# Optimization experiments

Measured on AMD Instinct MI355X. Metric: run time of the kernel, lower is better.

The kernel has to match this reference:

```python
import jax, jax.numpy as jnp
import numpy as np

D_MODEL = 512
N_HEADS = 8
HEAD_DIM = D_MODEL // N_HEADS
MAX_LEN = 250  # relative table has 2*MAX_LEN-1 = 499 rows
B, L = 2, 2048


def setup_inputs() -> dict:
    rng = jax.random.key(0)
    ks = jax.random.split(rng, 10)
    w = 1.0 / np.sqrt(D_MODEL)
    return {
        "query": jax.random.normal(ks[0], (B, L, D_MODEL), jnp.float32),
        "key": jax.random.normal(ks[1], (B, L, D_MODEL), jnp.float32),
        "value": jax.random.normal(ks[2], (B, L, D_MODEL), jnp.float32),
        "mask": jax.random.randint(ks[3], (B, L), 0, 2, jnp.int32),
        # weights stored as [in, out]; apply as x @ W + b (equivalent to torch Linear)
        "Wq": jax.random.normal(ks[4], (D_MODEL, D_MODEL), jnp.float32) * w,
        "bq": jnp.zeros((D_MODEL,), jnp.float32),
        "Wk": jax.random.normal(ks[5], (D_MODEL, D_MODEL), jnp.float32) * w,
        "bk": jnp.zeros((D_MODEL,), jnp.float32),
        "Wv": jax.random.normal(ks[6], (D_MODEL, D_MODEL), jnp.float32) * w,
        "bv": jnp.zeros((D_MODEL,), jnp.float32),
        "Wo": jax.random.normal(ks[7], (D_MODEL, D_MODEL), jnp.float32) * w,
        "bo": jnp.zeros((D_MODEL,), jnp.float32),
        "rel_table": jax.random.normal(ks[8], (2 * MAX_LEN - 1, HEAD_DIM), jnp.float32),
    }


def reference(query, key, value, mask, Wq, bq, Wk, bk, Wv, bv, Wo, bo, rel_table):
    b, l, d = query.shape
    hd = d // N_HEADS

    def split_heads(x):  # [b,l,d] -> [b,h,l,hd]
        return x.reshape(b, l, N_HEADS, hd).transpose(0, 2, 1, 3)

    Q = split_heads(query @ Wq + bq)
    K = split_heads(key @ Wk + bk)
    V = split_heads(value @ Wv + bv)

    scores = jnp.einsum('bhid,bhjd->bhij', Q, K) / jnp.sqrt(jnp.float32(hd))

    # relative position indices: idx[i,j] = clamp(j - i + MAX_LEN-1, 0, 2*MAX_LEN-2)
    pos = jnp.arange(l)
    idx = jnp.clip(pos[None, :] - pos[:, None] + MAX_LEN - 1, 0, 2 * MAX_LEN - 2)
    rel = rel_table[idx]  # [l, l, hd] gather
    # Shaw-style additive relative-position bias (per-pair scalar from Q . rel)
    scores = scores + jnp.einsum('bhid,ijd->bhij', Q, rel)

    # key-padding mask: [b,l] -> [b,1,1,l]
    scores = jnp.where(mask[:, None, None, :] == 0, jnp.float32(-1e10), scores)

    weights = jax.nn.softmax(scores, axis=-1)  # [b,h,l,l]
    out = jnp.einsum('bhij,bhjd->bhid', weights, V)
    out = out.transpose(0, 2, 1, 3).reshape(b, l, d)
    return out @ Wo + bo
```

## Files before the change

### kernel.cpp

```cpp
#include <hip/hip_runtime.h>
#include <math.h>

#define NREL 499
#define NREL_PAD 504
#define LDB 72
#define LDT 72

typedef __attribute__((ext_vector_type(8))) short bf16x8;
typedef __attribute__((ext_vector_type(4))) float f32x4;

__device__ __forceinline__ float bf2f(ushort x) {
  union { unsigned u; float f; } v; v.u = ((unsigned)x) << 16; return v.f;
}
__device__ __forceinline__ ushort f2bf(float x) {
  union { float f; unsigned u; } v; v.f = x;
  return (ushort)((v.u + 0x8000u) >> 16);
}
__device__ __forceinline__ ushort f2h(float x) {
  union { _Float16 h; ushort u; } v; v.h = (_Float16)x; return v.u;
}
__device__ __forceinline__ float h2f(ushort u) {
  union { _Float16 h; ushort u; } v; v.u = u; return (float)v.h;
}
__device__ __forceinline__ bf16x8 pack8(float4 a, float4 b) {
  bf16x8 r;
  r[0] = (short)f2bf(a.x); r[1] = (short)f2bf(a.y);
  r[2] = (short)f2bf(a.z); r[3] = (short)f2bf(a.w);
  r[4] = (short)f2bf(b.x); r[5] = (short)f2bf(b.y);
  r[6] = (short)f2bf(b.z); r[7] = (short)f2bf(b.w);
  return r;
}

__global__ __launch_bounds__(256) void prep_wt(const float* __restrict__ W0,
                                               const float* __restrict__ W1,
                                               const float* __restrict__ W2,
                                               const float* __restrict__ W3,
                                               const int* __restrict__ mask,
                                               const float* __restrict__ rel,
                                               ushort* __restrict__ Wt,
                                               ushort* __restrict__ maskbf,
                                               ushort* __restrict__ rel8) {
  __shared__ float T[64][68];
  const int t = threadIdx.x;
  const int k0 = blockIdx.x * 64, n0 = blockIdx.y * 64, z = blockIdx.z;
  const float* W = (z == 0) ? W0 : (z == 1) ? W1 : (z == 2) ? W2 : W3;
#pragma unroll
  for (int s = 0; s < 4; ++s) {
    int idx = t + s * 256;
    int r = idx >> 4, c4 = (idx & 15) << 2;
    *(float4*)&T[r][c4] = *(const float4*)(W + (size_t)(k0 + r) * 512 + n0 + c4);
  }
  if (blockIdx.x == 0 && blockIdx.y == 0) {
    int base = z * 1024 + t * 4;
    int4 mv = *(const int4*)(mask + base);
    ushort4 mo;
    mo.x = mv.x ? 0x3F80 : 0; mo.y = mv.y ? 0x3F80 : 0;
    mo.z = mv.z ? 0x3F80 : 0; mo.w = mv.w ? 0x3F80 : 0;
    *(ushort4*)(maskbf + base) = mo;
  } else if (blockIdx.x == 1 && blockIdx.y == 0) {
    int base = z * 8192 + t * 32;
#pragma unroll
    for (int c = 0; c < 4; ++c) {
      int e0 = base + c * 8;
      ushort tmp[8];
#pragma unroll
      for (int k = 0; k < 8; ++k) {
        int e = e0 + k;
        float v = (e < NREL * 64) ? rel[e] * 8.f : 0.f;
        tmp[k] = f2bf(v);
      }
      *(ushort4*)(rel8 + e0) = make_ushort4(tmp[0], tmp[1], tmp[2], tmp[3]);
      *(ushort4*)(rel8 + e0 + 4) = make_ushort4(tmp[4], tmp[5], tmp[6], tmp[7]);
    }
  }
  __syncthreads();
#pragma unroll
  for (int s = 0; s < 4; ++s) {
    int idx = t + s * 256;
    int row = idx >> 4, c4 = (idx & 15) << 2;
    ushort4 u = make_ushort4(f2bf(T[c4 + 0][row]), f2bf(T[c4 + 1][row]),
                             f2bf(T[c4 + 2][row]), f2bf(T[c4 + 3][row]));
    *(ushort4*)(Wt + (size_t)z * 262144 + (size_t)(n0 + row) * 512 + k0 + c4) = u;
  }
}

template <int MODE, int AFP32>
__device__ __forceinline__ void gemm_tile_body(const void* __restrict__ Av,
                                               const ushort* __restrict__ Wt,
                                               const float* __restrict__ bias,
                                               const int* __restrict__ mvec,
                                               void* __restrict__ outv,
                                               int bx, int by, float oscale) {
  __shared__ ushort As[64 * LDT];
  __shared__ ushort Bs[64 * LDT];
  const int t = threadIdx.x;
  const int lane = t & 63, wave = t >> 6;
  const int m16 = lane & 15, quad = lane >> 4;
  const int koff = quad << 3;
  const int i0 = by * 64, n0 = bx * 64;
  const int row0 = t >> 3, off0 = (t & 7) << 3;
  const int row1 = (t + 256) >> 3, off1 = ((t + 256) & 7) << 3;
  const ushort* Ab16 = (const ushort*)Av + (size_t)i0 * 512;
  const float*  Ab32 = (const float*)Av + (size_t)i0 * 512;
  const ushort* Bb = Wt + (size_t)n0 * 512;

  uint4 ar0, ar1;
  float4 af00, af01, af10, af11;
  if (AFP32) {
    af00 = *(const float4*)(Ab32 + (size_t)row0 * 512 + off0);
    af01 = *(const float4*)(Ab32 + (size_t)row0 * 512 + off0 + 4);
    af10 = *(const float4*)(Ab32 + (size_t)row1 * 512 + off1);
    af11 = *(const float4*)(Ab32 + (size_t)row1 * 512 + off1 + 4);
  } else {
    ar0 = *(const uint4*)(Ab16 + (size_t)row0 * 512 + off0);
    ar1 = *(const uint4*)(Ab16 + (size_t)row1 * 512 + off1);
  }
  uint4 br0 = *(const uint4*)(Bb + (size_t)row0 * 512 + off0);
  uint4 br1 = *(const uint4*)(Bb + (size_t)row1 * 512 + off1);

  f32x4 acc[4] = {{0.f, 0.f, 0.f, 0.f}, {0.f, 0.f, 0.f, 0.f},
                  {0.f, 0.f, 0.f, 0.f}, {0.f, 0.f, 0.f, 0.f}};

  for (int ks = 0; ks < 8; ++ks) {
    __syncthreads();
    if (AFP32) {
      *(bf16x8*)&As[row0 * LDT + off0] = pack8(af00, af01);
      *(bf16x8*)&As[row1 * LDT + off1] = pack8(af10, af11);
    } else {
      *(uint4*)&As[row0 * LDT + off0] = ar0;
      *(uint4*)&As[row1 * LDT + off1] = ar1;
    }
    *(uint4*)&Bs[row0 * LDT + off0] = br0;
    *(uint4*)&Bs[row1 * LDT + off1] = br1;
    __syncthreads();

    const int kn = ((ks + 1) & 7) << 6;
    if (AFP32) {
      af00 = *(const float4*)(Ab32 + (size_t)row0 * 512 + kn + off0);
      af01 = *(const float4*)(Ab32 + (size_t)row0 * 512 + kn + off0 + 4);
      af10 = *(const float4*)(Ab32 + (size_t)row1 * 512 + kn + off1);
      af11 = *(const float4*)(Ab32 + (size_t)row1 * 512 + kn + off1 + 4);
    } else {
      ar0 = *(const uint4*)(Ab16 + (size_t)row0 * 512 + kn + off0);
      ar1 = *(const uint4*)(Ab16 + (size_t)row1 * 512 + kn + off1);
    }
    br0 = *(const uint4*)(Bb + (size_t)row0 * 512 + kn + off0);
    br1 = *(const uint4*)(Bb + (size_t)row1 * 512 + kn + off1);

    __builtin_amdgcn_s_setprio(1);
    if (MODE != 1) {
#pragma unroll
      for (int kh = 0; kh < 2; ++kh) {
        bf16x8 af = *(const bf16x8*)&As[((wave << 4) + m16) * LDT + (kh << 5) + koff];
#pragma unroll
        for (int nt = 0; nt < 4; ++nt) {
          bf16x8 wf = *(const bf16x8*)&Bs[((nt << 4) + m16) * LDT + (kh << 5) + koff];
          acc[nt] = __builtin_amdgcn_mfma_f32_16x16x32_bf16(af, wf, acc[nt], 0, 0, 0);
        }
      }
    } else {
#pragma unroll
      for (int kh = 0; kh < 2; ++kh) {
        bf16x8 wf = *(const bf16x8*)&Bs[((wave << 4) + m16) * LDT + (kh << 5) + koff];
#pragma unroll
        for (int it = 0; it < 4; ++it) {
          bf16x8 af = *(const bf16x8*)&As[((it << 4) + m16) * LDT + (kh << 5) + koff];
          acc[it] = __builtin_amdgcn_mfma_f32_16x16x32_bf16(wf, af, acc[it], 0, 0, 0);
        }
      }
    }
    __builtin_amdgcn_s_setprio(0);
  }

  if (MODE == 0) {
    float* out = (float*)outv;
#pragma unroll
    for (int nt = 0; nt < 4; ++nt) {
      float bn = bias[n0 + (nt << 4) + m16];
#pragma unroll
      for (int r = 0; r < 4; ++r) {
        int i = i0 + (wave << 4) + (quad << 2) + r;
        out[(size_t)i * 512 + n0 + (nt << 4) + m16] = acc[nt][r] + bn;
      }
    }
  } else {
    ushort* out = (ushort*)outv;
    const int b = i0 >> 11, l0 = i0 & 2047, h = n0 >> 6;
    float4 b4 = *(const float4*)(bias + n0 + (wave << 4) + (quad << 2));
    float bb[4] = {b4.x, b4.y, b4.z, b4.w};
    float mkf[4];
#pragma unroll
    for (int it = 0; it < 4; ++it)
      mkf[it] = (mvec[b * 2048 + l0 + (it << 4) + m16] != 0) ? 1.f : 0.f;
#pragma unroll
    for (int r = 0; r < 4; ++r) {
      int d = (wave << 4) + (quad << 2) + r;
#pragma unroll
      for (int it = 0; it < 4; ++it) {
        out[((size_t)(b * 8 + h) * 64 + d) * 2048 + l0 + (it << 4) + m16] =
            f2bf((acc[it][r] + bb[r]) * mkf[it]);
      }
    }
  }
}

template <int MODE, int AFP32>
__global__ __launch_bounds__(256) void gemm_tile(const void* __restrict__ A,
                                                 const ushort* __restrict__ Wt,
                                                 const float* __restrict__ bias,
                                                 void* __restrict__ outv) {
  gemm_tile_body<MODE, AFP32>(A, Wt, bias, nullptr, outv, blockIdx.x,
                              blockIdx.y, 1.f);
}

template <int QREL>
__device__ __forceinline__ void gemm_qk128(const float* __restrict__ A,
                                           const ushort* __restrict__ Wt,
                                           const float* __restrict__ bias,
                                           ushort* __restrict__ out,
                                           const ushort* __restrict__ rel8,
                                           ushort* __restrict__ qrelh,
                                           int bx, int by, float oscale) {
  __shared__ ushort As[128 * LDT];
  __shared__ ushort Bs[64 * LDT];
  const int t = threadIdx.x;
  const int lane = t & 63, wave = t >> 6;
  const int m16 = lane & 15, quad = lane >> 4;
  const int koff = quad << 3;
  const int i0 = by * 128, n0 = bx * 64;
  const float* Ab = A + (size_t)i0 * 512;
  const ushort* Bb = Wt + (size_t)n0 * 512;

  int arow[4], acol[4];
#pragma unroll
  for (int s = 0; s < 4; ++s) {
    int idx = t + s * 256;
    arow[s] = idx >> 3;
    acol[s] = (idx & 7) << 3;
  }
  const int brow0 = t >> 3, bcol0 = (t & 7) << 3;
  const int brow1 = (t + 256) >> 3, bcol1 = ((t + 256) & 7) << 3;

  float4 afA[4], afB[4];
  uint4 br0, br1;
#pragma unroll
  for (int s = 0; s < 4; ++s) {
    afA[s] = *(const float4*)(Ab + (size_t)arow[s] * 512 + acol[s]);
    afB[s] = *(const float4*)(Ab + (size_t)arow[s] * 512 + acol[s] + 4);
  }
  br0 = *(const uint4*)(Bb + (size_t)brow0 * 512 + bcol0);
  br1 = *(const uint4*)(Bb + (size_t)brow1 * 512 + bcol1);

  f32x4 acc[2][4];
#pragma unroll
  for (int mi = 0; mi < 2; ++mi)
#pragma unroll
    for (int nt = 0; nt < 4; ++nt) acc[mi][nt] = (f32x4){0.f, 0.f, 0.f, 0.f};

  for (int ks = 0; ks < 8; ++ks) {
    __syncthreads();
#pragma unroll
    for (int s = 0; s < 4; ++s)
      *(bf16x8*)&As[arow[s] * LDT + acol[s]] = pack8(afA[s], afB[s]);
    *(uint4*)&Bs[brow0 * LDT + bcol0] = br0;
    *(uint4*)&Bs[brow1 * LDT + bcol1] = br1;
    __syncthreads();

    const int kn = ((ks + 1) & 7) << 6;
#pragma unroll
    for (int s = 0; s < 4; ++s) {
      afA[s] = *(const float4*)(Ab + (size_t)arow[s] * 512 + kn + acol[s]);
      afB[s] = *(const float4*)(Ab + (size_t)arow[s] * 512 + kn + acol[s] + 4);
    }
    br0 = *(const uint4*)(Bb + (size_t)brow0 * 512 + kn + bcol0);
    br1 = *(const uint4*)(Bb + (size_t)brow1 * 512 + kn + bcol1);

    __builtin_amdgcn_s_setprio(1);
#pragma unroll
    for (int kh = 0; kh < 2; ++kh) {
      bf16x8 af0 = *(const bf16x8*)&As[((wave << 5) + m16) * LDT + (kh << 5) + koff];
      bf16x8 af1 = *(const bf16x8*)&As[((wave << 5) + 16 + m16) * LDT + (kh << 5) + koff];
#pragma unroll
      for (int nt = 0; nt < 4; ++nt) {
        bf16x8 wf = *(const bf16x8*)&Bs[((nt << 4) + m16) * LDT + (kh << 5) + koff];
        acc[0][nt] = __builtin_amdgcn_mfma_f32_16x16x32_bf16(af0, wf, acc[0][nt], 0, 0, 0);
        acc[1][nt] = __builtin_amdgcn_mfma_f32_16x16x32_bf16(af1, wf, acc[1][nt], 0, 0, 0);
      }
    }
    __builtin_amdgcn_s_setprio(0);
  }

  const int b = i0 >> 11, l0 = i0 & 2047, h = n0 >> 6;
#pragma unroll
  for (int nt = 0; nt < 4; ++nt) {
    float bn = bias[n0 + (nt << 4) + m16];
    int d = (nt << 4) + m16;
#pragma unroll
    for (int mi = 0; mi < 2; ++mi) {
#pragma unroll
      for (int r = 0; r < 4; ++r) {
        int il = (wave << 5) + (mi << 4) + (quad << 2) + r;
        ushort qb = f2bf((acc[mi][nt][r] + bn) * oscale);
        out[((size_t)(b * 8 + h) * 2048 + l0 + il) * 64 + d] = qb;
        if (QREL) As[il * LDT + d] = qb;
      }
    }
  }

  if (QREL) {
    __asm__ volatile("s_waitcnt lgkmcnt(0)" ::: "memory");
    bf16x8 afq[2][2];
#pragma unroll
    for (int g = 0; g < 2; ++g)
#pragma unroll
      for (int kh = 0; kh < 2; ++kh)
        afq[g][kh] = *(const bf16x8*)&As[((wave << 5) + (g << 4) + m16) * LDT +
                                         (kh << 5) + koff];
    const int bh = b * 8 + h;
    for (int rc = 0; rc < 32; ++rc) {
      const ushort* rp = rel8 + (size_t)((rc << 4) + m16) * 64;
      bf16x8 wf0 = *(const bf16x8*)(rp + koff);
      bf16x8 wf1 = *(const bf16x8*)(rp + 32 + koff);
      int r = (rc << 4) + m16;
#pragma unroll
      for (int g = 0; g < 2; ++g) {
        f32x4 aq = {0.f, 0.f, 0.f, 0.f};
        aq = __builtin_amdgcn_mfma_f32_16x16x32_bf16(afq[g][0], wf0, aq, 0, 0, 0);
        aq = __builtin_amdgcn_mfma_f32_16x16x32_bf16(afq[g][1], wf1, aq, 0, 0, 0);
        if (r < NREL_PAD) {
#pragma unroll
          for (int rg = 0; rg < 4; ++rg) {
            int l = l0 + (wave << 5) + (g << 4) + (quad << 2) + rg;
            qrelh[((size_t)bh * 2048 + l) * NREL_PAD + r] = f2h(aq[rg]);
          }
        }
      }
    }
  }
}

__global__ __launch_bounds__(256) void gemm_qkv(
    const float* __restrict__ q, const float* __restrict__ k,
    const float* __restrict__ v, const ushort* __restrict__ Wt,
    const float* __restrict__ bq, const float* __restrict__ bk,
    const float* __restrict__ bv, const int* __restrict__ mask,
    const ushort* __restrict__ rel8, ushort* __restrict__ Qw,
    ushort* __restrict__ Kw, ushort* __restrict__ Vtw,
    ushort* __restrict__ qrelh) {
  const int z = blockIdx.z;
  if (z == 0) {
    gemm_qk128<1>(q, Wt, bq, Qw, rel8, qrelh, blockIdx.x, blockIdx.y, 0.125f);
  } else if (z == 1) {
    gemm_qk128<0>(k, Wt + 262144, bk, Kw, nullptr, nullptr, blockIdx.x,
                  blockIdx.y, 1.f);
  } else {
#pragma unroll
    for (int s = 0; s < 2; ++s)
      gemm_tile_body<1, 1>(v, Wt + 2 * 262144, bv, mask, (void*)Vtw,
                           blockIdx.x, blockIdx.y * 2 + s, 1.f);
  }
}

__device__ __forceinline__ void gather_qv(float qv[4][4],
                                          const ushort* __restrict__ qrow,
                                          float e_lo, float e_hi,
                                          int iq, int iw0, int j0, int quad) {
  if (j0 - iw0 >= 264) {
#pragma unroll
    for (int jt = 0; jt < 4; ++jt)
#pragma unroll
      for (int r = 0; r < 4; ++r) qv[jt][r] = e_hi;
  } else if (iw0 - j0 >= 312) {
#pragma unroll
    for (int jt = 0; jt < 4; ++jt)
#pragma unroll
      for (int r = 0; r < 4; ++r) qv[jt][r] = e_lo;
  } else {
#pragma unroll
    for (int jt = 0; jt < 4; ++jt) {
#pragma unroll
      for (int r = 0; r < 4; ++r) {
        int j = j0 + (jt << 4) + (quad << 2) + r;
        int rr = min(NREL - 1, max(0, j - iq + 249));
        qv[jt][r] = h2f(qrow[rr]);
      }
    }
  }
}

__global__ __launch_bounds__(256) void flash_attn(
    const ushort* __restrict__ Qw, const ushort* __restrict__ Kw,
    const ushort* __restrict__ Vt, const ushort* __restrict__ qrelh,
    const ushort* __restrict__ maskbf, ushort* __restrict__ attnbf) {
  __shared__ ushort QPs[64 * LDB];
  __shared__ ushort Ks[64 * LDB];
  __shared__ ushort Vs[64 * LDB];
  const int t = threadIdx.x;
  const int lane = t & 63, wave = t >> 6;
  const int m16 = lane & 15, quad = lane >> 4;
  const int koff = quad << 3;
  const int bid = ((int)blockIdx.y << 5) + (int)blockIdx.x;
  const int swz = ((bid & 7) << 6) + (bid >> 3);
  const int i0 = (swz & 31) << 6;
  const int bh = swz >> 5;
  const int b = bh >> 3, h = bh & 7;
  const ushort* Qb = Qw + (size_t)bh * 2048 * 64;
  const ushort* Kb = Kw + (size_t)bh * 2048 * 64;
  const ushort* Vb = Vt + (size_t)bh * 64 * 2048;
  const ushort* mbf = maskbf + b * 2048;
  const int iw0 = i0 + (wave << 4);
  const int iq = iw0 + m16;
  const ushort* qrow = qrelh + ((size_t)bh * 2048 + iq) * NREL_PAD;
  const float e_lo = h2f(qrow[0]), e_hi = h2f(qrow[NREL - 1]);

  const int row0 = t >> 3, off0 = (t & 7) << 3;
  const int row1 = (t + 256) >> 3, off1 = ((t + 256) & 7) << 3;

  *(uint4*)&QPs[row0 * LDB + off0] =
      *(const uint4*)(Qb + (size_t)(i0 + row0) * 64 + off0);
  *(uint4*)&QPs[row1 * LDB + off1] =
      *(const uint4*)(Qb + (size_t)(i0 + row1) * 64 + off1);
  __syncthreads();

  bf16x8 qa0 = *(const bf16x8*)&QPs[((wave << 4) + m16) * LDB + koff];
  bf16x8 qa1 = *(const bf16x8*)&QPs[((wave << 4) + m16) * LDB + 32 + koff];

  float m_i = -INFINITY;
  f32x4 oacc[4];
  f32x4 lacc = {0.f, 0.f, 0.f, 0.f};
#pragma unroll
  for (int dt = 0; dt < 4; ++dt) oacc[dt] = (f32x4){0.f, 0.f, 0.f, 0.f};

  uint4 krA0 = *(const uint4*)(Kb + (size_t)row0 * 64 + off0);
  uint4 krA1 = *(const uint4*)(Kb + (size_t)row1 * 64 + off1);
  uint4 vrA0 = *(const uint4*)(Vb + (size_t)row0 * 2048 + off0);
  uint4 vrA1 = *(const uint4*)(Vb + (size_t)row1 * 2048 + off1);
  bf16x8 mfA0 = *(const bf16x8*)(mbf + koff);
  bf16x8 mfA1 = *(const bf16x8*)(mbf + 32 + koff);
  float qvA[4][4];
  gather_qv(qvA, qrow, e_lo, e_hi, iq, iw0, 0, quad);
  uint4 krB0, krB1, vrB0, vrB1;
  bf16x8 mfB0, mfB1;
  float qvB[4][4];

#define FLASH_STEP(KR0, KR1, VR0, VR1, MF0, MF1, QV,                          \
                   KN0, KN1, VN0, VN1, MG0, MG1, QN, JN)                      \
  do {                                                                        \
    __syncthreads();                                                          \
    *(uint4*)&Ks[row0 * LDB + off0] = KR0;                                    \
    *(uint4*)&Ks[row1 * LDB + off1] = KR1;                                    \
    *(uint4*)&Vs[row0 * LDB + off0] = VR0;                                    \
    *(uint4*)&Vs[row1 * LDB + off1] = VR1;                                    \
    __syncthreads();                                                          \
    KN0 = *(const uint4*)(Kb + (size_t)((JN) + row0) * 64 + off0);            \
    KN1 = *(const uint4*)(Kb + (size_t)((JN) + row1) * 64 + off1);            \
    VN0 = *(const uint4*)(Vb + (size_t)row0 * 2048 + (JN) + off0);            \
    VN1 = *(const uint4*)(Vb + (size_t)row1 * 2048 + (JN) + off1);            \
    MG0 = *(const bf16x8*)(mbf + (JN) + koff);                                \
    MG1 = *(const bf16x8*)(mbf + (JN) + 32 + koff);                           \
    gather_qv(QN, qrow, e_lo, e_hi, iq, iw0, (JN), quad);                     \
    f32x4 sacc[4];                                                            \
    __builtin_amdgcn_s_setprio(1);                                            \
    _Pragma("unroll")                                                         \
    for (int jt = 0; jt < 4; ++jt) {                                          \
      bf16x8 kf0 = *(const bf16x8*)&Ks[((jt << 4) + m16) * LDB + koff];       \
      bf16x8 kf1 = *(const bf16x8*)&Ks[((jt << 4) + m16) * LDB + 32 + koff];  \
      f32x4 z = {QV[jt][0], QV[jt][1], QV[jt][2], QV[jt][3]};                 \
      z = __builtin_amdgcn_mfma_f32_16x16x32_bf16(kf0, qa0, z, 0, 0, 0);      \
      z = __builtin_amdgcn_mfma_f32_16x16x32_bf16(kf1, qa1, z, 0, 0, 0);      \
      sacc[jt] = z;                                                           \
    }                                                                         \
    __builtin_amdgcn_s_setprio(0);                                            \
    float t0 = fmaxf(fmaxf(sacc[0][0], sacc[0][1]),                           \
                     fmaxf(sacc[0][2], sacc[0][3]));                          \
    float t1 = fmaxf(fmaxf(sacc[1][0], sacc[1][1]),                           \
                     fmaxf(sacc[1][2], sacc[1][3]));                          \
    float t2 = fmaxf(fmaxf(sacc[2][0], sacc[2][1]),                           \
                     fmaxf(sacc[2][2], sacc[2][3]));                          \
    float t3 = fmaxf(fmaxf(sacc[3][0], sacc[3][1]),                           \
                     fmaxf(sacc[3][2], sacc[3][3]));                          \
    float mx = fmaxf(fmaxf(t0, t1), fmaxf(t2, t3));                           \
    mx = fmaxf(mx, __shfl_xor(mx, 16));                                       \
    mx = fmaxf(mx, __shfl_xor(mx, 32));                                       \
    if (__any(mx > m_i + 8.f)) {                                              \
      float mnew = fmaxf(m_i, mx);                                            \
      float al = __expf(m_i - mnew);                                          \
      m_i = mnew;                                                             \
      _Pragma("unroll")                                                       \
      for (int dt = 0; dt < 4; ++dt) {                                        \
        oacc[dt][0] *= al; oacc[dt][1] *= al;                                 \
        oacc[dt][2] *= al; oacc[dt][3] *= al;                                 \
      }                                                                       \
      lacc[0] *= al; lacc[1] *= al; lacc[2] *= al; lacc[3] *= al;             \
    }                                                                         \
    const int prow = ((wave << 4) + m16) * LDB;                               \
    _Pragma("unroll")                                                         \
    for (int jt = 0; jt < 4; ++jt) {                                          \
      ushort4 pk;                                                             \
      pk.x = f2bf(__expf(sacc[jt][0] - m_i));                                 \
      pk.y = f2bf(__expf(sacc[jt][1] - m_i));                                 \
      pk.z = f2bf(__expf(sacc[jt][2] - m_i));                                 \
      pk.w = f2bf(__expf(sacc[jt][3] - m_i));                                 \
      *(ushort4*)&QPs[prow + (jt << 4) + (quad << 2)] = pk;                   \
    }                                                                         \
    __asm__ volatile("s_waitcnt lgkmcnt(0)" ::: "memory");                    \
    bf16x8 pa0 = *(const bf16x8*)&QPs[prow + koff];                           \
    bf16x8 pa1 = *(const bf16x8*)&QPs[prow + 32 + koff];                      \
    __builtin_amdgcn_s_setprio(1);                                            \
    lacc = __builtin_amdgcn_mfma_f32_16x16x32_bf16(MF0, pa0, lacc, 0, 0, 0);  \
    lacc = __builtin_amdgcn_mfma_f32_16x16x32_bf16(MF1, pa1, lacc, 0, 0, 0);  \
    _Pragma("unroll")                                                         \
    for (int dt = 0; dt < 4; ++dt) {                                          \
      bf16x8 vf0 = *(const bf16x8*)&Vs[((dt << 4) + m16) * LDB + koff];       \
      bf16x8 vf1 = *(const bf16x8*)&Vs[((dt << 4) + m16) * LDB + 32 + koff];  \
      oacc[dt] =                                                              \
          __builtin_amdgcn_mfma_f32_16x16x32_bf16(vf0, pa0, oacc[dt], 0, 0, 0); \
      oacc[dt] =                                                              \
          __builtin_amdgcn_mfma_f32_16x16x32_bf16(vf1, pa1, oacc[dt], 0, 0, 0); \
    }                                                                         \
    __builtin_amdgcn_s_setprio(0);                                            \
  } while (0)

  for (int j0 = 0; j0 < 2048; j0 += 128) {
    FLASH_STEP(krA0, krA1, vrA0, vrA1, mfA0, mfA1, qvA,
               krB0, krB1, vrB0, vrB1, mfB0, mfB1, qvB, j0 + 64);
    FLASH_STEP(krB0, krB1, vrB0, vrB1, mfB0, mfB1, qvB,
               krA0, krA1, vrA0, vrA1, mfA0, mfA1, qvA, (j0 + 128) & 2047);
  }
#undef FLASH_STEP

  float inv = 1.0f / lacc[0];
  ushort* dst = attnbf + (size_t)(b * 2048 + iq) * 512 + h * 64;
#pragma unroll
  for (int dt = 0; dt < 4; ++dt) {
    ushort4 st;
    st.x = f2bf(oacc[dt][0] * inv);
    st.y = f2bf(oacc[dt][1] * inv);
    st.z = f2bf(oacc[dt][2] * inv);
    st.w = f2bf(oacc[dt][3] * inv);
    *(ushort4*)(dst + (dt << 4) + (quad << 2)) = st;
  }
}

extern "C" void kernel_launch(void* const* d_in, const int* in_sizes, int n_in,
                              void* d_out, int out_size, void* d_ws,
                              size_t ws_size, hipStream_t stream) {
  const float* query = (const float*)d_in[0];
  const float* key   = (const float*)d_in[1];
  const float* value = (const float*)d_in[2];
  const int*   mask  = (const int*)d_in[3];
  const float* Wq = (const float*)d_in[4];
  const float* bq = (const float*)d_in[5];
  const float* Wk = (const float*)d_in[6];
  const float* bk = (const float*)d_in[7];
  const float* Wv = (const float*)d_in[8];
  const float* bv = (const float*)d_in[9];
  const float* Wo = (const float*)d_in[10];
  const float* bo = (const float*)d_in[11];
  const float* rel = (const float*)d_in[12];

  char* w = (char*)d_ws;
  size_t off = 0;
  ushort* Qw  = (ushort*)(w + off); off += (size_t)16 * 2048 * 64 * 2;
  ushort* Kw  = (ushort*)(w + off); off += (size_t)16 * 2048 * 64 * 2;
  ushort* Vtw = (ushort*)(w + off); off += (size_t)16 * 64 * 2048 * 2;
  ushort* Wt  = (ushort*)(w + off); off += (size_t)4 * 512 * 512 * 2;
  ushort* qrelh = (ushort*)(w + off); off += (size_t)16 * 2048 * NREL_PAD * 2;
  ushort* attnbf = (ushort*)(w + off); off += (size_t)4096 * 512 * 2;
  ushort* maskbf = (ushort*)(w + off); off += (size_t)2 * 2048 * 2;
  ushort* rel8 = (ushort*)(w + off); off += (size_t)512 * 64 * 2;
  float* out = (float*)d_out;

  dim3 bb(256);
  hipLaunchKernelGGL(prep_wt, dim3(8, 8, 4), bb, 0, stream, Wq, Wk, Wv, Wo,
                     mask, rel, Wt, maskbf, rel8);
  hipLaunchKernelGGL(gemm_qkv, dim3(8, 32, 3), bb, 0, stream, query, key, value,
                     Wt, bq, bk, bv, mask, rel8, Qw, Kw, Vtw, qrelh);
  hipLaunchKernelGGL(flash_attn, dim3(32, 16), bb, 0, stream, Qw, Kw, Vtw,
                     qrelh, maskbf, attnbf);
  hipLaunchKernelGGL((gemm_tile<0, 0>), dim3(8, 64), bb, 0, stream, attnbf,
                     Wt + 3 * 262144, bo, (void*)out);
}
```

Baseline: 205.5 us.

## Double-buffer K/V tiles in LDS to drop one barrier per step

K and V now get two LDS buffers. Each step writes the next tile into the idle buffer while computing on the current one, and global loads are issued two tiles ahead. This removes one of the two __syncthreads per iteration and lets LDS stores overlap with MFMA work. The cost is twice the LDS for K/V, which may reduce occupancy, plus extra register pressure.

```diff
diff --git a/kernel.cpp b/kernel.cpp
--- a/kernel.cpp
+++ b/kernel.cpp
@@ -5,6 +5,7 @@
 #define NREL_PAD 504
 #define LDB 72
 #define LDT 72
+#define KVSZ (64 * LDB)
 
 typedef __attribute__((ext_vector_type(8))) short bf16x8;
 typedef __attribute__((ext_vector_type(4))) float f32x4;
@@ -393,8 +394,8 @@
     const ushort* __restrict__ Vt, const ushort* __restrict__ qrelh,
     const ushort* __restrict__ maskbf, ushort* __restrict__ attnbf) {
   __shared__ ushort QPs[64 * LDB];
-  __shared__ ushort Ks[64 * LDB];
-  __shared__ ushort Vs[64 * LDB];
+  __shared__ ushort Ks[2 * KVSZ];
+  __shared__ ushort Vs[2 * KVSZ];
   const int t = threadIdx.x;
   const int lane = t & 63, wave = t >> 6;
   const int m16 = lane & 15, quad = lane >> 4;
@@ -420,51 +421,64 @@
       *(const uint4*)(Qb + (size_t)(i0 + row0) * 64 + off0);
   *(uint4*)&QPs[row1 * LDB + off1] =
       *(const uint4*)(Qb + (size_t)(i0 + row1) * 64 + off1);
+
+  uint4 kr0 = *(const uint4*)(Kb + (size_t)row0 * 64 + off0);
+  uint4 kr1 = *(const uint4*)(Kb + (size_t)row1 * 64 + off1);
+  uint4 vr0 = *(const uint4*)(Vb + (size_t)row0 * 2048 + off0);
+  uint4 vr1 = *(const uint4*)(Vb + (size_t)row1 * 2048 + off1);
   __syncthreads();
 
   bf16x8 qa0 = *(const bf16x8*)&QPs[((wave << 4) + m16) * LDB + koff];
   bf16x8 qa1 = *(const bf16x8*)&QPs[((wave << 4) + m16) * LDB + 32 + koff];
 
-  float m_i = -INFINITY;
-  f32x4 oacc[4];
-  f32x4 lacc = {0.f, 0.f, 0.f, 0.f};
-#pragma unroll
-  for (int dt = 0; dt < 4; ++dt) oacc[dt] = (f32x4){0.f, 0.f, 0.f, 0.f};
-
-  uint4 krA0 = *(const uint4*)(Kb + (size_t)row0 * 64 + off0);
-  uint4 krA1 = *(const uint4*)(Kb + (size_t)row1 * 64 + off1);
-  uint4 vrA0 = *(const uint4*)(Vb + (size_t)row0 * 2048 + off0);
-  uint4 vrA1 = *(const uint4*)(Vb + (size_t)row1 * 2048 + off1);
+  *(uint4*)&Ks[row0 * LDB + off0] = kr0;
+  *(uint4*)&Ks[row1 * LDB + off1] = kr1;
+  *(uint4*)&Vs[row0 * LDB + off0] = vr0;
+  *(uint4*)&Vs[row1 * LDB + off1] = vr1;
+  kr0 = *(const uint4*)(Kb + (size_t)(64 + row0) * 64 + off0);
+  kr1 = *(const uint4*)(Kb + (size_t)(64 + row1) * 64 + off1);
+  vr0 = *(const uint4*)(Vb + (size_t)row0 * 2048 + 64 + off0);
+  vr1 = *(const uint4*)(Vb + (size_t)row1 * 2048 + 64 + off1);
+
   bf16x8 mfA0 = *(const bf16x8*)(mbf + koff);
   bf16x8 mfA1 = *(const bf16x8*)(mbf + 32 + koff);
   float qvA[4][4];
   gather_qv(qvA, qrow, e_lo, e_hi, iq, iw0, 0, quad);
-  uint4 krB0, krB1, vrB0, vrB1;
   bf16x8 mfB0, mfB1;
   float qvB[4][4];
 
-#define FLASH_STEP(KR0, KR1, VR0, VR1, MF0, MF1, QV,                          \
-                   KN0, KN1, VN0, VN1, MG0, MG1, QN, JN)                      \
+  float m_i = -INFINITY;
+  f32x4 oacc[4];
+  f32x4 lacc = {0.f, 0.f, 0.f, 0.f};
+#pragma unroll
+  for (int dt = 0; dt < 4; ++dt) oacc[dt] = (f32x4){0.f, 0.f, 0.f, 0.f};
+
+  __syncthreads();
+
+#define FLASH_STEP(CUR, NXT, QV, MF0, MF1, QN, MG0, MG1, JN1, JN2)            \
   do {                                                                        \
-    __syncthreads();                                                          \
-    *(uint4*)&Ks[row0 * LDB + off0] = KR0;                                    \
-    *(uint4*)&Ks[row1 * LDB + off1] = KR1;                                    \
-    *(uint4*)&Vs[row0 * LDB + off0] = VR0;                                    \
-    *(uint4*)&Vs[row1 * LDB + off1] = VR1;                                    \
-    __syncthreads();                                                          \
-    KN0 = *(const uint4*)(Kb + (size_t)((JN) + row0) * 64 + off0);            \
-    KN1 = *(const uint4*)(Kb + (size_t)((JN) + row1) * 64 + off1);            \
-    VN0 = *(const uint4*)(Vb + (size_t)row0 * 2048 + (JN) + off0);            \
-    VN1 = *(const uint4*)(Vb + (size_t)row1 * 2048 + (JN) + off1);            \
-    MG0 = *(const bf16x8*)(mbf + (JN) + koff);                                \
-    MG1 = *(const bf16x8*)(mbf + (JN) + 32 + koff);                           \
-    gather_qv(QN, qrow, e_lo, e_hi, iq, iw0, (JN), quad);                     \
+           \
+    *(uint4*)&Ks[(NXT) + row0 * LDB + off0] = kr0;                            \
+    *(uint4*)&Ks[(NXT) + row1 * LDB + off1] = kr1;                            \
+    *(uint4*)&Vs[(NXT) + row0 * LDB + off0] = vr0;                            \
+    *(uint4*)&Vs[(NXT) + row1 * LDB + off1] = vr1;                            \
+                            \
+    kr0 = *(const uint4*)(Kb + (size_t)((JN2) + row0) * 64 + off0);           \
+    kr1 = *(const uint4*)(Kb + (size_t)((JN2) + row1) * 64 + off1);           \
+    vr0 = *(const uint4*)(Vb + (size_t)row0 * 2048 + (JN2) + off0);           \
+    vr1 = *(const uint4*)(Vb + (size_t)row1 * 2048 + (JN2) + off1);           \
+                                         \
+    MG0 = *(const bf16x8*)(mbf + (JN1) + koff);                               \
+    MG1 = *(const bf16x8*)(mbf + (JN1) + 32 + koff);                          \
+    gather_qv(QN, qrow, e_lo, e_hi, iq, iw0, (JN1), quad);                    \
+                                    \
     f32x4 sacc[4];                                                            \
     __builtin_amdgcn_s_setprio(1);                                            \
     _Pragma("unroll")                                                         \
     for (int jt = 0; jt < 4; ++jt) {                                          \
-      bf16x8 kf0 = *(const bf16x8*)&Ks[((jt << 4) + m16) * LDB + koff];       \
-      bf16x8 kf1 = *(const bf16x8*)&Ks[((jt << 4) + m16) * LDB + 32 + koff];  \
+      bf16x8 kf0 = *(const bf16x8*)&Ks[(CUR) + ((jt << 4) + m16) * LDB + koff]; \
+      bf16x8 kf1 =                                                            \
+          *(const bf16x8*)&Ks[(CUR) + ((jt << 4) + m16) * LDB + 32 + koff];   \
       f32x4 z = {QV[jt][0], QV[jt][1], QV[jt][2], QV[jt][3]};                 \
       z = __builtin_amdgcn_mfma_f32_16x16x32_bf16(kf0, qa0, z, 0, 0, 0);      \
       z = __builtin_amdgcn_mfma_f32_16x16x32_bf16(kf1, qa1, z, 0, 0, 0);      \
@@ -511,21 +525,24 @@
     lacc = __builtin_amdgcn_mfma_f32_16x16x32_bf16(MF1, pa1, lacc, 0, 0, 0);  \
     _Pragma("unroll")                                                         \
     for (int dt = 0; dt < 4; ++dt) {                                          \
-      bf16x8 vf0 = *(const bf16x8*)&Vs[((dt << 4) + m16) * LDB + koff];       \
-      bf16x8 vf1 = *(const bf16x8*)&Vs[((dt << 4) + m16) * LDB + 32 + koff];  \
+      bf16x8 vf0 =                                                            \
+          *(const bf16x8*)&Vs[(CUR) + ((dt << 4) + m16) * LDB + koff];        \
+      bf16x8 vf1 =                                                            \
+          *(const bf16x8*)&Vs[(CUR) + ((dt << 4) + m16) * LDB + 32 + koff];   \
       oacc[dt] =                                                              \
           __builtin_amdgcn_mfma_f32_16x16x32_bf16(vf0, pa0, oacc[dt], 0, 0, 0); \
       oacc[dt] =                                                              \
           __builtin_amdgcn_mfma_f32_16x16x32_bf16(vf1, pa1, oacc[dt], 0, 0, 0); \
     }                                                                         \
     __builtin_amdgcn_s_setprio(0);                                            \
+    __syncthreads();             \
   } while (0)
 
   for (int j0 = 0; j0 < 2048; j0 += 128) {
-    FLASH_STEP(krA0, krA1, vrA0, vrA1, mfA0, mfA1, qvA,
-               krB0, krB1, vrB0, vrB1, mfB0, mfB1, qvB, j0 + 64);
-    FLASH_STEP(krB0, krB1, vrB0, vrB1, mfB0, mfB1, qvB,
-               krA0, krA1, vrA0, vrA1, mfA0, mfA1, qvA, (j0 + 128) & 2047);
+    FLASH_STEP(0, KVSZ, qvA, mfA0, mfA1, qvB, mfB0, mfB1,
+               j0 + 64, (j0 + 128) & 2047);
+    FLASH_STEP(KVSZ, 0, qvB, mfB0, mfB1, qvA, mfA0, mfA1,
+               (j0 + 128) & 2047, (j0 + 192) & 2047);
   }
 #undef FLASH_STEP
 
```

Result: no change. 205.6 us, median of 2 (+0.0%).
